# Kernel optimization log

Hardware: AMD Instinct MI355X
Metric: run time of the kernel (lower is better)

Reference implementation:

```python
import jax, jax.numpy as jnp
import numpy as np

B = 4096
N0 = 784          # MNIST input
L0 = 263          # fc0: Gather chain 784 -> 256 (ELU after each)
L2 = 121          # fc2: Gather chain 256 -> 12 (ELU after each); final Gather 12 -> 10 has no ELU


def _win3(x):
    # x: (B, N) -> (B, N-2, 3) sliding windows of width 3
    return jnp.stack([x[:, :-2], x[:, 1:-1], x[:, 2:]], axis=-1)


def setup_inputs() -> dict:
    key = jax.random.key(0)
    kx, k0, k1, k2, k3, k4 = jax.random.split(key, 6)
    s = 0.75  # keeps activation variance roughly stable through ~380 ELU glia layers
    x = jax.random.normal(kx, (B, N0), jnp.float32)
    W0 = jax.random.normal(k0, (L0, 782, 3), jnp.float32) * s
    m0 = np.arange(782)[None, :] < (780 - 2 * np.arange(L0))[:, None]
    W0 = W0 * jnp.asarray(m0[..., None], jnp.float32)  # zero out rows past each layer's out size
    Ws = jax.random.normal(k1, (256, 3), jnp.float32) * s
    bs = jax.random.normal(k2, (256,), jnp.float32) * 0.1
    W2 = jax.random.normal(k3, (L2, 254, 3), jnp.float32) * s
    m2 = np.arange(254)[None, :] < (252 - 2 * np.arange(L2))[:, None]
    W2 = W2 * jnp.asarray(m2[..., None], jnp.float32)
    Wlast = jax.random.normal(k4, (10, 3), jnp.float32) * s
    return {"x": x, "W0": W0, "Ws": Ws, "bs": bs, "W2": W2, "Wlast": Wlast}


def reference(x, W0, Ws, bs, W2, Wlast):
    def gather_step(h, W):
        # locally-connected width-3 Gather (out = in - 2, bias=False) + ELU.
        # Invalid tail rows of W are zero, so padded positions stay exactly 0
        # (ELU(0)=0) and never contaminate valid windows.
        y = jax.nn.elu(jnp.einsum('bjk,jk->bj', _win3(h), W))
        return jnp.pad(y, ((0, 0), (0, 2))), None

    # fc0: 263 Gather+ELU layers, 784 -> 256 (valid prefix of fixed-width state)
    h, _ = jax.lax.scan(gather_step, x, W0)
    h = h[:, :256]
    # fc1: Slide(256) + ELU -- same-size width-3 locally connected layer, zero-padded window, bias
    hp = jnp.pad(h, ((0, 0), (1, 1)))
    h = jax.nn.elu(jnp.einsum('bjk,jk->bj', _win3(hp), Ws) + bs)
    # fc2: 121 Gather+ELU layers, 256 -> 12
    h, _ = jax.lax.scan(gather_step, h, W2)
    # final Gather(12): 12 -> 10, no ELU
    logits = jnp.einsum('bjk,jk->bj', _win3(h[:, :12]), Wlast)
    return jax.nn.log_softmax(logits, axis=1)
```

## Files before the change

### kernel.cpp

```cpp
#include <hip/hip_runtime.h>
#include <math.h>


#define G 2

template<int HI>
__device__ __forceinline__ float2 pk_mul_b(float2 a, float2 w) {
    float2 d;
    if constexpr (HI)
        asm("v_pk_mul_f32 %0, %1, %2 op_sel:[0,1] op_sel_hi:[1,1]"
            : "=v"(d) : "v"(a), "v"(w));
    else
        asm("v_pk_mul_f32 %0, %1, %2 op_sel_hi:[1,0]"
            : "=v"(d) : "v"(a), "v"(w));
    return d;
}
template<int HI>
__device__ __forceinline__ float2 pk_fma_b(float2 a, float2 w, float2 c) {
    float2 d;
    if constexpr (HI)
        asm("v_pk_fma_f32 %0, %1, %2, %3 op_sel:[0,1,0] op_sel_hi:[1,1,1]"
            : "=v"(d) : "v"(a), "v"(w), "v"(c));
    else
        asm("v_pk_fma_f32 %0, %1, %2, %3 op_sel_hi:[1,0,1]"
            : "=v"(d) : "v"(a), "v"(w), "v"(c));
    return d;
}
__device__ __forceinline__ float2 pk_mul2(float2 a, float2 b) {
    float2 d;
    asm("v_pk_mul_f32 %0, %1, %2" : "=v"(d) : "v"(a), "v"(b));
    return d;
}
__device__ __forceinline__ float vexp2(float x) {
    float d;
    asm("v_exp_f32 %0, %1" : "=v"(d) : "v"(x));
    return d;
}

__device__ __forceinline__ float elu_f(float a) {
    return a > 0.0f ? a : (__expf(a) - 1.0f);
}

template<int K, int I, int NW>
__device__ __forceinline__ void slot_run(float2 (&h)[K], const float2 (&w)[NW],
                                         float2 e0, float2 e1, float2 l2e) {
    if constexpr (I < K) {
        float2 x1, x2;
        if constexpr (I + 1 < K) x1 = h[I + 1]; else x1 = e0;
        if constexpr (I + 2 < K) x2 = h[I + 2];
        else if constexpr (I + 2 == K) x2 = e0;
        else x2 = e1;
        float2 acc = pk_mul_b<(3 * I + 2) & 1>(x2, w[(3 * I + 2) >> 1]);
        acc = pk_fma_b<(3 * I + 1) & 1>(x1, w[(3 * I + 1) >> 1], acc);
        acc = pk_fma_b<(3 * I) & 1>(h[I], w[(3 * I) >> 1], acc);
        float2 t = pk_mul2(acc, l2e);
        float ex = vexp2(t.x) - 1.0f;
        float ey = vexp2(t.y) - 1.0f;
        h[I].x = acc.x > 0.0f ? acc.x : ex;
        h[I].y = acc.y > 0.0f ? acc.y : ey;
        slot_run<K, I + 1, NW>(h, w, e0, e1, l2e);
    }
}

template<int K, int NW>
__device__ __forceinline__ void scan_layer_pk(float2 (&h)[K], const float2 (&w)[NW],
                                              float2 l2e) {
    float2 e0, e1;
    e0.x = __shfl_down(h[0].x, 1); e0.y = __shfl_down(h[0].y, 1);
    if constexpr (K >= 2) { e1.x = __shfl_down(h[1].x, 1); e1.y = __shfl_down(h[1].y, 1); }
    else                  { e1.x = __shfl_down(h[0].x, 2); e1.y = __shfl_down(h[0].y, 2); }
    slot_run<K, 0, NW>(h, w, e0, e1, l2e);
}

template<int NC>
__device__ __forceinline__ void load_wt2(float2 (&w)[2 * NC], const float4* __restrict__ Tp,
                                         int lr) {
#pragma unroll
    for (int c = 0; c < NC; ++c) {
        float4 v = Tp[(size_t)lr * (NC * 64) + c * 64];
        w[2 * c]     = make_float2(v.x, v.y);
        w[2 * c + 1] = make_float2(v.z, v.w);
    }
}

template<int K, int NC, int NL>
__device__ __forceinline__ void scan_phase_pk(const float* __restrict__ Tphase,
                                              int lane, float2 (&h)[K], float2 l2e) {
    const float4* __restrict__ Tp = reinterpret_cast<const float4*>(Tphase) + lane;
    float2 wa[2 * NC], wb[2 * NC];
    load_wt2<NC>(wa, Tp, 0);
    int l = 0;
    for (; l + 2 <= NL; l += 2) {
        load_wt2<NC>(wb, Tp, l + 1);
        __builtin_amdgcn_sched_barrier(0);
        scan_layer_pk<K>(h, wa, l2e);
        load_wt2<NC>(wa, Tp, l + 2);
        __builtin_amdgcn_sched_barrier(0);
        scan_layer_pk<K>(h, wb, l2e);
    }
    if constexpr (NL % 2 == 1) scan_layer_pk<K>(h, wa, l2e);
}

template<int KA, int KB>
__device__ __forceinline__ void repack_pk(float2 (&a)[KA], float2 (&n)[KB],
                                          float2* lds, int lane) {
    __syncthreads();
#pragma unroll
    for (int i = 0; i < KA; ++i) lds[KA * lane + i] = a[i];
    __syncthreads();
#pragma unroll
    for (int i = 0; i < KB; ++i) n[i] = lds[KB * lane + i];
    __syncthreads();
}

__device__ __forceinline__ void stage2_pk(float2 (&h)[5], const float* __restrict__ Ws,
                                          const float* __restrict__ bs, int lane) {
#pragma unroll
    for (int i = 0; i < 5; ++i)
        if (5 * lane + i > 255) h[i] = make_float2(0.f, 0.f);
    float w0[5], w1[5], w2[5], bb[5];
#pragma unroll
    for (int i = 0; i < 5; ++i) {
        int j = 5 * lane + i;
        bool v = j < 256;
        w0[i] = v ? Ws[3 * j + 0] : 0.f;
        w1[i] = v ? Ws[3 * j + 1] : 0.f;
        w2[i] = v ? Ws[3 * j + 2] : 0.f;
        bb[i] = v ? bs[j] : 0.f;
    }
    float2 p, q;
    p.x = __shfl_up(h[4].x, 1); p.y = __shfl_up(h[4].y, 1);
    if (lane == 0) p = make_float2(0.f, 0.f);
    q.x = __shfl_down(h[0].x, 1); q.y = __shfl_down(h[0].y, 1);
    float2 y[5];
#pragma unroll
    for (int i = 0; i < 5; ++i) {
        float2 xm = (i == 0) ? p : h[i - 1];
        float2 xp = (i == 4) ? q : h[i + 1];
        float ax = fmaf(xm.x, w0[i], fmaf(h[i].x, w1[i], fmaf(xp.x, w2[i], bb[i])));
        float ay = fmaf(xm.y, w0[i], fmaf(h[i].y, w1[i], fmaf(xp.y, w2[i], bb[i])));
        y[i].x = elu_f(ax);
        y[i].y = elu_f(ay);
    }
#pragma unroll
    for (int i = 0; i < 5; ++i) h[i] = y[i];
}

__device__ __forceinline__ void emit_row(float v, const float* __restrict__ Wl,
                                         float* __restrict__ out, int row, int lane) {
    float n1 = __shfl_down(v, 1);
    float n2 = __shfl_down(v, 2);
    float lg = 0.0f;
    if (lane < 10)
        lg = fmaf(v, Wl[3 * lane], fmaf(n1, Wl[3 * lane + 1], n2 * Wl[3 * lane + 2]));
    float t = (lane < 10) ? lg : -1e30f;
#pragma unroll
    for (int d = 1; d < 16; d <<= 1) t = fmaxf(t, __shfl_xor(t, d));
    float e = (lane < 10) ? __expf(lg - t) : 0.0f;
    float s = e;
#pragma unroll
    for (int d = 1; d < 16; d <<= 1) s += __shfl_xor(s, d);
    float lse = t + __logf(s);
    if (lane < 10) out[(size_t)row * 10 + lane] = lg - lse;
}

#define T_TOTAL 531712
#define T_ALLOC (T_TOTAL + 512)

__global__ __launch_bounds__(256)
void reorder_w(const float* __restrict__ W0, const float* __restrict__ W2,
               float* __restrict__ T) {
    int idx = blockIdx.x * 256 + threadIdx.x;
    if (idx >= T_ALLOC) return;
    if (idx >= T_TOTAL) { T[idx] = 0.0f; return; }
    int base, l0, K, NC, s1;
    if      (idx < 17920)  { base = 0;      l0 = 0;   K = 13; NC = 10; s1 = 1; }
    else if (idx < 91648)  { base = 17920;  l0 = 7;   K = 12; NC = 9;  s1 = 1; }
    else if (idx < 165376) { base = 91648;  l0 = 39;  K = 11; NC = 9;  s1 = 1; }
    else if (idx < 230912) { base = 165376; l0 = 71;  K = 10; NC = 8;  s1 = 1; }
    else if (idx < 288256) { base = 230912; l0 = 103; K = 9;  NC = 7;  s1 = 1; }
    else if (idx < 337408) { base = 288256; l0 = 135; K = 8;  NC = 6;  s1 = 1; }
    else if (idx < 386560) { base = 337408; l0 = 167; K = 7;  NC = 6;  s1 = 1; }
    else if (idx < 427520) { base = 386560; l0 = 199; K = 6;  NC = 5;  s1 = 1; }
    else if (idx < 460288) { base = 427520; l0 = 231; K = 5;  NC = 4;  s1 = 1; }
    else if (idx < 484096) { base = 460288; l0 = 0;   K = 4;  NC = 3;  s1 = 0; }
    else if (idx < 508672) { base = 484096; l0 = 31;  K = 3;  NC = 3;  s1 = 0; }
    else if (idx < 525056) { base = 508672; l0 = 63;  K = 2;  NC = 2;  s1 = 0; }
    else                   { base = 525056; l0 = 95;  K = 1;  NC = 1;  s1 = 0; }
    const float* Wsrc = s1 ? W0 : W2;
    int lstride = s1 ? 2346 : 762;
    int rel  = idx - base;
    int perL = NC * 256;
    int lr   = rel / perL;
    int r2   = rel - lr * perL;
    int c    = r2 >> 8;
    int ln   = (r2 >> 2) & 63;
    int f    = r2 & 3;
    int elem = 4 * c + f;
    float v = 0.0f;
    if (elem < 3 * K) {
        int b = 3 * K * ln;
        if (b + 3 * K > lstride) b = lstride - 3 * K;
        v = Wsrc[(size_t)(l0 + lr) * lstride + b + elem];
    }
    T[idx] = v;
}

__global__ __launch_bounds__(64)
void pg_kernel_pk(const float* __restrict__ x,  const float* __restrict__ Ws,
                  const float* __restrict__ bs, const float* __restrict__ Wlast,
                  const float* __restrict__ T,  float* __restrict__ out)
{
    __shared__ float2 lds2[13 * 64];
    const int lane = threadIdx.x;
    const int rowA = blockIdx.x * G;
    const int rowB = rowA + 1;
    const float2 l2e = make_float2(1.44269504088896340736f, 1.44269504088896340736f);

    float2 h13[13];
#pragma unroll
    for (int i = 0; i < 13; ++i) {
        int p = 13 * lane + i;
        h13[i].x = (p < 784) ? x[(size_t)rowA * 784 + p] : 0.0f;
        h13[i].y = (p < 784) ? x[(size_t)rowB * 784 + p] : 0.0f;
    }

    scan_phase_pk<13, 10, 7>(T + 0,       lane, h13, l2e);
    float2 h12[12]; repack_pk<13, 12>(h13, h12, lds2, lane);
    scan_phase_pk<12, 9, 32>(T + 17920,   lane, h12, l2e);
    float2 h11[11]; repack_pk<12, 11>(h12, h11, lds2, lane);
    scan_phase_pk<11, 9, 32>(T + 91648,   lane, h11, l2e);
    float2 h10[10]; repack_pk<11, 10>(h11, h10, lds2, lane);
    scan_phase_pk<10, 8, 32>(T + 165376,  lane, h10, l2e);
    float2 h9[9];   repack_pk<10, 9>(h10, h9, lds2, lane);
    scan_phase_pk<9, 7, 32>(T + 230912,   lane, h9, l2e);
    float2 h8[8];   repack_pk<9, 8>(h9, h8, lds2, lane);
    scan_phase_pk<8, 6, 32>(T + 288256,   lane, h8, l2e);
    float2 h7[7];   repack_pk<8, 7>(h8, h7, lds2, lane);
    scan_phase_pk<7, 6, 32>(T + 337408,   lane, h7, l2e);
    float2 h6[6];   repack_pk<7, 6>(h7, h6, lds2, lane);
    scan_phase_pk<6, 5, 32>(T + 386560,   lane, h6, l2e);
    float2 h5[5];   repack_pk<6, 5>(h6, h5, lds2, lane);
    scan_phase_pk<5, 4, 32>(T + 427520,   lane, h5, l2e);

    stage2_pk(h5, Ws, bs, lane);

    float2 h4[4];   repack_pk<5, 4>(h5, h4, lds2, lane);
    scan_phase_pk<4, 3, 31>(T + 460288,   lane, h4, l2e);
    float2 h3[3];   repack_pk<4, 3>(h4, h3, lds2, lane);
    scan_phase_pk<3, 3, 32>(T + 484096,   lane, h3, l2e);
    float2 h2[2];   repack_pk<3, 2>(h3, h2, lds2, lane);
    scan_phase_pk<2, 2, 32>(T + 508672,   lane, h2, l2e);
    float2 h1[1];   repack_pk<2, 1>(h2, h1, lds2, lane);
    scan_phase_pk<1, 1, 26>(T + 525056,   lane, h1, l2e);

    emit_row(h1[0].x, Wlast, out, rowA, lane);
    emit_row(h1[0].y, Wlast, out, rowB, lane);
}

template<int K>
__device__ __forceinline__ void scan_layer_s(float (&h)[K], const float (&w)[3 * K]) {
    float e0 = __shfl_down(h[0], 1);
    float e1;
    if constexpr (K >= 2) e1 = __shfl_down(h[1], 1);
    else                  e1 = __shfl_down(h[0], 2);
#pragma unroll
    for (int i = 0; i < K; ++i) {
        float x1 = (i + 1 < K) ? h[i + 1] : e0;
        float x2 = (i + 2 < K) ? h[i + 2] : ((i + 2 == K) ? e0 : e1);
        float a = fmaf(h[i], w[3 * i], fmaf(x1, w[3 * i + 1], x2 * w[3 * i + 2]));
        h[i] = elu_f(a);
    }
}
template<int K>
__device__ __forceinline__ void scan_phase_s(const float* __restrict__ W, int lstride,
                                             int l0, int l1, int lane,
                                             float (&hA)[K], float (&hB)[K]) {
    int base = 3 * K * lane;
    if (base + 3 * K > lstride) base = lstride - 3 * K;
    const float* __restrict__ Wp = W + (size_t)l0 * lstride + base;
    float wa[3 * K];
    for (int l = l0; l < l1; ++l) {
#pragma unroll
        for (int j = 0; j < 3 * K; ++j) wa[j] = Wp[j];
        scan_layer_s<K>(hA, wa);
        scan_layer_s<K>(hB, wa);
        Wp += lstride;
    }
}
template<int KA, int KB>
__device__ __forceinline__ void repack_s(float (&aA)[KA], float (&aB)[KA],
                                         float (&nA)[KB], float (&nB)[KB],
                                         float* lds, int lane) {
    __syncthreads();
#pragma unroll
    for (int i = 0; i < KA; ++i) lds[KA * lane + i] = aA[i];
    __syncthreads();
#pragma unroll
    for (int i = 0; i < KB; ++i) nA[i] = lds[KB * lane + i];
    __syncthreads();
#pragma unroll
    for (int i = 0; i < KA; ++i) lds[KA * lane + i] = aB[i];
    __syncthreads();
#pragma unroll
    for (int i = 0; i < KB; ++i) nB[i] = lds[KB * lane + i];
    __syncthreads();
}
__global__ __launch_bounds__(64)
void pg_kernel_d(const float* __restrict__ x,  const float* __restrict__ W0,
                 const float* __restrict__ Ws, const float* __restrict__ bs,
                 const float* __restrict__ W2, const float* __restrict__ Wlast,
                 float* __restrict__ out)
{
    __shared__ float lds[13 * 64];
    const int lane = threadIdx.x;
    const int rowA = blockIdx.x * 2;
    const int rowB = rowA + 1;
    float a13[13], b13[13];
#pragma unroll
    for (int i = 0; i < 13; ++i) {
        int p = 13 * lane + i;
        a13[i] = (p < 784) ? x[(size_t)rowA * 784 + p] : 0.0f;
        b13[i] = (p < 784) ? x[(size_t)rowB * 784 + p] : 0.0f;
    }
    scan_phase_s<13>(W0, 2346, 0, 71, lane, a13, b13);
    float a10[10], b10[10]; repack_s<13, 10>(a13, b13, a10, b10, lds, lane);
    scan_phase_s<10>(W0, 2346, 71, 167, lane, a10, b10);
    float a7[7], b7[7];     repack_s<10, 7>(a10, b10, a7, b7, lds, lane);
    scan_phase_s<7>(W0, 2346, 167, 231, lane, a7, b7);
    float a5[5], b5[5];     repack_s<7, 5>(a7, b7, a5, b5, lds, lane);
    scan_phase_s<5>(W0, 2346, 231, 263, lane, a5, b5);
    {
        float2 hp[5];
#pragma unroll
        for (int i = 0; i < 5; ++i) hp[i] = make_float2(a5[i], b5[i]);
        stage2_pk(hp, Ws, bs, lane);
#pragma unroll
        for (int i = 0; i < 5; ++i) { a5[i] = hp[i].x; b5[i] = hp[i].y; }
    }
    float a4[4], b4[4];     repack_s<5, 4>(a5, b5, a4, b4, lds, lane);
    scan_phase_s<4>(W2, 762, 0, 31, lane, a4, b4);
    float a3[3], b3[3];     repack_s<4, 3>(a4, b4, a3, b3, lds, lane);
    scan_phase_s<3>(W2, 762, 31, 63, lane, a3, b3);
    float a2_[2], b2_[2];   repack_s<3, 2>(a3, b3, a2_, b2_, lds, lane);
    scan_phase_s<2>(W2, 762, 63, 95, lane, a2_, b2_);
    float a1[1], b1[1];     repack_s<2, 1>(a2_, b2_, a1, b1, lds, lane);
    scan_phase_s<1>(W2, 762, 95, 121, lane, a1, b1);
    emit_row(a1[0], Wlast, out, rowA, lane);
    emit_row(b1[0], Wlast, out, rowB, lane);
}

extern "C" void kernel_launch(void* const* d_in, const int* in_sizes, int n_in,
                              void* d_out, int out_size, void* d_ws, size_t ws_size,
                              hipStream_t stream) {
    const float* x     = (const float*)d_in[0];
    const float* W0    = (const float*)d_in[1];
    const float* Ws    = (const float*)d_in[2];
    const float* bs    = (const float*)d_in[3];
    const float* W2    = (const float*)d_in[4];
    const float* Wlast = (const float*)d_in[5];
    float* out = (float*)d_out;

    if (ws_size >= (size_t)T_ALLOC * sizeof(float)) {
        float* T = (float*)d_ws;
        reorder_w<<<(T_ALLOC + 255) / 256, 256, 0, stream>>>(W0, W2, T);
        pg_kernel_pk<<<4096 / G, 64, 0, stream>>>(x, Ws, bs, Wlast, T, out);
    } else {
        pg_kernel_d<<<2048, 64, 0, stream>>>(x, W0, Ws, bs, W2, Wlast, out);
    }
}
```

Baseline: 247.0 us.

## Stream layer weights through LDS double buffer via global_load_lds, drop barriers

```diff
diff --git a/kernel.cpp b/kernel.cpp
--- a/kernel.cpp
+++ b/kernel.cpp
@@ -3,6 +3,7 @@
 
 
 #define G 2
+#define BUFF4 576
 
 template<int HI>
 __device__ __forceinline__ float2 pk_mul_b(float2 a, float2 w) {
@@ -36,9 +37,20 @@
     asm("v_exp_f32 %0, %1" : "=v"(d) : "v"(x));
     return d;
 }
+__device__ __forceinline__ float med3z(float a, float em1) {
+    float d;
+    asm("v_med3_f32 %0, %1, %2, 0" : "=v"(d) : "v"(a), "v"(em1));
+    return d;
+}
 
 __device__ __forceinline__ float elu_f(float a) {
     return a > 0.0f ? a : (__expf(a) - 1.0f);
+}
+
+__device__ __forceinline__ void gl2lds16(const float4* g, float4* l) {
+    __builtin_amdgcn_global_load_lds(
+        (const __attribute__((address_space(1))) unsigned int*)(const void*)g,
+        (__attribute__((address_space(3))) unsigned int*)(void*)l, 16, 0, 0);
 }
 
 template<int K, int I, int NW>
@@ -56,8 +68,8 @@
         float2 t = pk_mul2(acc, l2e);
         float ex = vexp2(t.x) - 1.0f;
         float ey = vexp2(t.y) - 1.0f;
-        h[I].x = acc.x > 0.0f ? acc.x : ex;
-        h[I].y = acc.y > 0.0f ? acc.y : ey;
+        h[I].x = med3z(acc.x, ex);
+        h[I].y = med3z(acc.y, ey);
         slot_run<K, I + 1, NW>(h, w, e0, e1, l2e);
     }
 }
@@ -84,33 +96,67 @@
 }
 
 template<int K, int NC, int NL>
-__device__ __forceinline__ void scan_phase_pk(const float* __restrict__ Tphase,
-                                              int lane, float2 (&h)[K], float2 l2e) {
-    const float4* __restrict__ Tp = reinterpret_cast<const float4*>(Tphase) + lane;
-    float2 wa[2 * NC], wb[2 * NC];
-    load_wt2<NC>(wa, Tp, 0);
-    int l = 0;
-    for (; l + 2 <= NL; l += 2) {
-        load_wt2<NC>(wb, Tp, l + 1);
+__device__ __forceinline__ void scan_direct(const float* __restrict__ Tph, int lane,
+                                            float2 (&h)[K], float2 l2e) {
+    const float4* __restrict__ Tp = reinterpret_cast<const float4*>(Tph) + lane;
+    for (int l = 0; l < NL; ++l) {
+        float2 w[2 * NC];
+        load_wt2<NC>(w, Tp, l);
+        scan_layer_pk<K>(h, w, l2e);
+    }
+}
+
+template<int NC>
+__device__ __forceinline__ void prefetch_layer0(const float* __restrict__ Tph, int lane,
+                                                float4* dst) {
+    const float4* src = reinterpret_cast<const float4*>(Tph) + lane;
+#pragma unroll
+    for (int c = 0; c < NC; ++c) gl2lds16(src + c * 64, dst + c * 64);
+}
+
+template<int K, int NC, int NL, int NNC>
+__device__ __forceinline__ void scan_phase_lds(const float* __restrict__ Tph,
+                                               const float* __restrict__ Tnext,
+                                               int lane, float2 (&h)[K], float2 l2e,
+                                               float4* pool, int& cur) {
+    const float4* __restrict__ Tp = reinterpret_cast<const float4*>(Tph) + lane;
+    for (int l = 0; l < NL; ++l) {
+        float4* dst = pool + (cur ^ 1) * BUFF4;
+        if (l + 1 < NL) {
+            const float4* src = Tp + (size_t)(l + 1) * (NC * 64);
+#pragma unroll
+            for (int c = 0; c < NC; ++c) gl2lds16(src + c * 64, dst + c * 64);
+        } else if constexpr (NNC > 0) {
+            const float4* src = reinterpret_cast<const float4*>(Tnext) + lane;
+#pragma unroll
+            for (int c = 0; c < NNC; ++c) gl2lds16(src + c * 64, dst + c * 64);
+        }
+        const float4* wsrc = pool + cur * BUFF4 + lane;
+        float2 w[2 * NC];
+#pragma unroll
+        for (int c = 0; c < NC; ++c) {
+            float4 v = wsrc[(size_t)c * 64];
+            w[2 * c]     = make_float2(v.x, v.y);
+            w[2 * c + 1] = make_float2(v.z, v.w);
+        }
+        scan_layer_pk<K>(h, w, l2e);
+        asm volatile("s_waitcnt vmcnt(0)" ::: "memory");
         __builtin_amdgcn_sched_barrier(0);
-        scan_layer_pk<K>(h, wa, l2e);
-        load_wt2<NC>(wa, Tp, l + 2);
-        __builtin_amdgcn_sched_barrier(0);
-        scan_layer_pk<K>(h, wb, l2e);
-    }
-    if constexpr (NL % 2 == 1) scan_layer_pk<K>(h, wa, l2e);
+        cur ^= 1;
+    }
 }
 
 template<int KA, int KB>
-__device__ __forceinline__ void repack_pk(float2 (&a)[KA], float2 (&n)[KB],
-                                          float2* lds, int lane) {
-    __syncthreads();
-#pragma unroll
-    for (int i = 0; i < KA; ++i) lds[KA * lane + i] = a[i];
-    __syncthreads();
-#pragma unroll
-    for (int i = 0; i < KB; ++i) n[i] = lds[KB * lane + i];
-    __syncthreads();
+__device__ __forceinline__ void repack_w(float2 (&a)[KA], float2 (&n)[KB],
+                                         float2* scratch, int lane) {
+#pragma unroll
+    for (int i = 0; i < KA; ++i) scratch[KA * lane + i] = a[i];
+    asm volatile("s_waitcnt lgkmcnt(0)" ::: "memory");
+    __builtin_amdgcn_sched_barrier(0);
+#pragma unroll
+    for (int i = 0; i < KB; ++i) n[i] = scratch[KB * lane + i];
+    asm volatile("s_waitcnt lgkmcnt(0)" ::: "memory");
+    __builtin_amdgcn_sched_barrier(0);
 }
 
 __device__ __forceinline__ void stage2_pk(float2 (&h)[5], const float* __restrict__ Ws,
@@ -211,7 +257,7 @@
                   const float* __restrict__ bs, const float* __restrict__ Wlast,
                   const float* __restrict__ T,  float* __restrict__ out)
 {
-    __shared__ float2 lds2[13 * 64];
+    __shared__ float4 pool[2 * BUFF4];
     const int lane = threadIdx.x;
     const int rowA = blockIdx.x * G;
     const int rowB = rowA + 1;
@@ -225,34 +271,40 @@
         h13[i].y = (p < 784) ? x[(size_t)rowB * 784 + p] : 0.0f;
     }
 
-    scan_phase_pk<13, 10, 7>(T + 0,       lane, h13, l2e);
-    float2 h12[12]; repack_pk<13, 12>(h13, h12, lds2, lane);
-    scan_phase_pk<12, 9, 32>(T + 17920,   lane, h12, l2e);
-    float2 h11[11]; repack_pk<12, 11>(h12, h11, lds2, lane);
-    scan_phase_pk<11, 9, 32>(T + 91648,   lane, h11, l2e);
-    float2 h10[10]; repack_pk<11, 10>(h11, h10, lds2, lane);
-    scan_phase_pk<10, 8, 32>(T + 165376,  lane, h10, l2e);
-    float2 h9[9];   repack_pk<10, 9>(h10, h9, lds2, lane);
-    scan_phase_pk<9, 7, 32>(T + 230912,   lane, h9, l2e);
-    float2 h8[8];   repack_pk<9, 8>(h9, h8, lds2, lane);
-    scan_phase_pk<8, 6, 32>(T + 288256,   lane, h8, l2e);
-    float2 h7[7];   repack_pk<8, 7>(h8, h7, lds2, lane);
-    scan_phase_pk<7, 6, 32>(T + 337408,   lane, h7, l2e);
-    float2 h6[6];   repack_pk<7, 6>(h7, h6, lds2, lane);
-    scan_phase_pk<6, 5, 32>(T + 386560,   lane, h6, l2e);
-    float2 h5[5];   repack_pk<6, 5>(h6, h5, lds2, lane);
-    scan_phase_pk<5, 4, 32>(T + 427520,   lane, h5, l2e);
+    scan_direct<13, 10, 7>(T + 0, lane, h13, l2e);
+    int cur = 0;
+    prefetch_layer0<9>(T + 17920, lane, pool + 0);
+    float2 h12[12];
+    repack_w<13, 12>(h13, h12, (float2*)(pool + BUFF4), lane);
+    asm volatile("s_waitcnt vmcnt(0)" ::: "memory");
+    __builtin_amdgcn_sched_barrier(0);
+
+    scan_phase_lds<12, 9, 32, 9>(T + 17920,  T + 91648,  lane, h12, l2e, pool, cur);
+    float2 h11[11]; repack_w<12, 11>(h12, h11, (float2*)(pool + (cur ^ 1) * BUFF4), lane);
+    scan_phase_lds<11, 9, 32, 8>(T + 91648,  T + 165376, lane, h11, l2e, pool, cur);
+    float2 h10[10]; repack_w<11, 10>(h11, h10, (float2*)(pool + (cur ^ 1) * BUFF4), lane);
+    scan_phase_lds<10, 8, 32, 7>(T + 165376, T + 230912, lane, h10, l2e, pool, cur);
+    float2 h9[9];   repack_w<10, 9>(h10, h9, (float2*)(pool + (cur ^ 1) * BUFF4), lane);
+    scan_phase_lds<9, 7, 32, 6>(T + 230912,  T + 288256, lane, h9, l2e, pool, cur);
+    float2 h8[8];   repack_w<9, 8>(h9, h8, (float2*)(pool + (cur ^ 1) * BUFF4), lane);
+    scan_phase_lds<8, 6, 32, 6>(T + 288256,  T + 337408, lane, h8, l2e, pool, cur);
+    float2 h7[7];   repack_w<8, 7>(h8, h7, (float2*)(pool + (cur ^ 1) * BUFF4), lane);
+    scan_phase_lds<7, 6, 32, 5>(T + 337408,  T + 386560, lane, h7, l2e, pool, cur);
+    float2 h6[6];   repack_w<7, 6>(h7, h6, (float2*)(pool + (cur ^ 1) * BUFF4), lane);
+    scan_phase_lds<6, 5, 32, 4>(T + 386560,  T + 427520, lane, h6, l2e, pool, cur);
+    float2 h5[5];   repack_w<6, 5>(h6, h5, (float2*)(pool + (cur ^ 1) * BUFF4), lane);
+    scan_phase_lds<5, 4, 32, 3>(T + 427520,  T + 460288, lane, h5, l2e, pool, cur);
 
     stage2_pk(h5, Ws, bs, lane);
 
-    float2 h4[4];   repack_pk<5, 4>(h5, h4, lds2, lane);
-    scan_phase_pk<4, 3, 31>(T + 460288,   lane, h4, l2e);
-    float2 h3[3];   repack_pk<4, 3>(h4, h3, lds2, lane);
-    scan_phase_pk<3, 3, 32>(T + 484096,   lane, h3, l2e);
-    float2 h2[2];   repack_pk<3, 2>(h3, h2, lds2, lane);
-    scan_phase_pk<2, 2, 32>(T + 508672,   lane, h2, l2e);
-    float2 h1[1];   repack_pk<2, 1>(h2, h1, lds2, lane);
-    scan_phase_pk<1, 1, 26>(T + 525056,   lane, h1, l2e);
+    float2 h4[4];   repack_w<5, 4>(h5, h4, (float2*)(pool + (cur ^ 1) * BUFF4), lane);
+    scan_phase_lds<4, 3, 31, 3>(T + 460288,  T + 484096, lane, h4, l2e, pool, cur);
+    float2 h3[3];   repack_w<4, 3>(h4, h3, (float2*)(pool + (cur ^ 1) * BUFF4), lane);
+    scan_phase_lds<3, 3, 32, 2>(T + 484096,  T + 508672, lane, h3, l2e, pool, cur);
+    float2 h2[2];   repack_w<3, 2>(h3, h2, (float2*)(pool + (cur ^ 1) * BUFF4), lane);
+    scan_phase_lds<2, 2, 32, 1>(T + 508672,  T + 525056, lane, h2, l2e, pool, cur);
+    float2 h1[1];   repack_w<2, 1>(h2, h1, (float2*)(pool + (cur ^ 1) * BUFF4), lane);
+    scan_phase_lds<1, 1, 26, 0>(T + 525056,  (const float*)0, lane, h1, l2e, pool, cur);
 
     emit_row(h1[0].x, Wlast, out, rowA, lane);
     emit_row(h1[0].y, Wlast, out, rowB, lane);
```

Result: slower. 277.8 us (+12.5%).
